# Performance work log

Measured on AMD Instinct MI355X. Metric: run time of the kernel, lower is better.

Reference implementation:

```python
import jax, jax.numpy as jnp
import numpy as np

IN_DIM = 4096
OUT_DIM = 2048
K = 4
R = 4096
B = 4096


def setup_inputs() -> dict:
    key = jax.random.key(0)
    ks = jax.random.split(key, 8)
    s = 0.02
    return {
        "hidden_states": jax.random.normal(ks[0], (B, IN_DIM), jnp.float32),
        # stacked per-block weights, torch Linear layout: W1/W3 [k+1, out, in], W2 [k+1, in, out]
        "W1": jax.random.normal(ks[1], (K + 1, OUT_DIM, IN_DIM), jnp.float32) * s,
        "W3": jax.random.normal(ks[2], (K + 1, OUT_DIM, IN_DIM), jnp.float32) * s,
        "W2": jax.random.normal(ks[3], (K + 1, IN_DIM, OUT_DIM), jnp.float32) * s,
        "fc1_w": jax.random.normal(ks[4], (R, IN_DIM * K), jnp.float32) * s,
        "fc1_b": jax.random.normal(ks[5], (R,), jnp.float32) * s,
        "fc2_w": jax.random.normal(ks[6], (IN_DIM, R), jnp.float32) * s,
        "fc2_b": jax.random.normal(ks[7], (IN_DIM,), jnp.float32) * s,
    }


def reference(hidden_states, W1, W3, W2, fc1_w, fc1_b, fc2_w, fc2_b):
    x = hidden_states
    # batched SwiGLU over k+1 blocks: [B, k+1, out]
    g = jax.nn.silu(jnp.einsum("bi,koi->bko", x, W1)) * jnp.einsum("bi,koi->bko", x, W3)
    wk_outs = jnp.einsum("bko,kio->bki", g, W2)  # [B, k+1, in]
    o0 = wk_outs[:, 0]                            # [B, in]
    concat = wk_outs[:, 1:].reshape(x.shape[0], -1)  # [B, k*in], matches torch.cat order
    h = jax.nn.silu(concat @ fc1_w.T + fc1_b)
    proj = h @ fc2_w.T + fc2_b                    # [B, in]
    diff = o0 - proj
    return (jnp.linalg.norm(diff, ord=2, axis=1), jnp.mean(jnp.abs(diff), axis=1))
```

## Files before the change

kernel.cpp:

```cpp
#include <hip/hip_runtime.h>
#include <hip/hip_bf16.h>
#include <cstdint>
#include <cstddef>

#define IN_DIM 4096
#define OUT_DIM 2048
#define NEXP 5
#define KEXP 4
#define RDIM 4096
#define BATCH 4096

typedef __hip_bfloat16 bf16;
typedef __attribute__((ext_vector_type(8))) short bf16x8;
typedef __attribute__((ext_vector_type(4))) float f32x4;
typedef __attribute__((ext_vector_type(8))) unsigned short u16x8;
typedef __attribute__((ext_vector_type(4))) unsigned short u16x4;

typedef const __attribute__((address_space(1))) unsigned int* as1p;
typedef __attribute__((address_space(3))) unsigned int* as3p;

__device__ __forceinline__ unsigned short f2bf(float x) {
  union { __hip_bfloat16 h; unsigned short u; } cv;
  cv.h = __float2bfloat16(x);
  return cv.u;
}

__global__ __launch_bounds__(256) void cvt_kernel(const float* __restrict__ in,
                                                  unsigned short* __restrict__ out,
                                                  int n8) {
  int i = blockIdx.x * 256 + threadIdx.x;
  if (i >= n8) return;
  const float4* p = (const float4*)in;
  float4 a = p[(size_t)i * 2];
  float4 b = p[(size_t)i * 2 + 1];
  u16x8 v;
  v[0] = f2bf(a.x); v[1] = f2bf(a.y); v[2] = f2bf(a.z); v[3] = f2bf(a.w);
  v[4] = f2bf(b.x); v[5] = f2bf(b.y); v[6] = f2bf(b.z); v[7] = f2bf(b.w);
  *(u16x8*)(out + (size_t)i * 8) = v;
}

__global__ __launch_bounds__(256) void tcvt_kernel(const float* __restrict__ in,
                                                   unsigned short* __restrict__ out,
                                                   int NI, int NO) {
  __shared__ float tile[32][33];
  const float* inz = in + (size_t)blockIdx.z * NI * NO;
  unsigned short* outz = out + (size_t)blockIdx.z * NI * NO;
  int i0 = blockIdx.y * 32;
  int o0 = blockIdx.x * 32;
  int t = threadIdx.x;
  int ri = t >> 3, ro = (t & 7) << 2;
  float4 v = *(const float4*)(inz + (size_t)(i0 + ri) * NO + o0 + ro);
  tile[ri][ro] = v.x; tile[ri][ro + 1] = v.y; tile[ri][ro + 2] = v.z; tile[ri][ro + 3] = v.w;
  __syncthreads();
  int wo = t >> 3, wi = (t & 7) << 2;
  u16x4 w;
  w[0] = f2bf(tile[wi][wo]);
  w[1] = f2bf(tile[wi + 1][wo]);
  w[2] = f2bf(tile[wi + 2][wo]);
  w[3] = f2bf(tile[wi + 3][wo]);
  *(u16x4*)(outz + (size_t)(o0 + wo) * NI + i0 + wi) = w;
}

__device__ __forceinline__ void gload16(const bf16* g, bf16* l) {
  __builtin_amdgcn_global_load_lds((as1p)g, (as3p)l, 16, 0, 0);
}

template <int N> __device__ __forceinline__ void vwait() {
  if constexpr (N == 0) asm volatile("s_waitcnt vmcnt(0)" ::: "memory");
  else if constexpr (N == 2) asm volatile("s_waitcnt vmcnt(2)" ::: "memory");
  else if constexpr (N == 4) asm volatile("s_waitcnt vmcnt(4)" ::: "memory");
}

#define READ_A(buf, mh)                                              \
  do {                                                               \
    const bf16* _pa = ldsA + (buf) * 16384 + (mh) * 8192;            \
    _Pragma("unroll") for (int m2 = 0; m2 < 4; ++m2) {               \
      afr[m2][0] = *(const bf16x8*)(_pa + aOff[m2]);                 \
      afr[m2][1] = *(const bf16x8*)(_pa + (aOff[m2] ^ 32));          \
    }                                                                \
  } while (0)

#define READ_B(buf, nh)                                              \
  do {                                                               \
    const bf16* _pb = ldsB + (buf) * 16384 + (nh) * 8192;            \
    _Pragma("unroll") for (int n2 = 0; n2 < 2; ++n2) {               \
      bfr[(nh) * 2 + n2][0] = *(const bf16x8*)(_pb + bOff[(nh) * 2 + n2]);        \
      bfr[(nh) * 2 + n2][1] = *(const bf16x8*)(_pb + (bOff[(nh) * 2 + n2] ^ 32)); \
    }                                                                \
  } while (0)

#define QMFMA(mh, nh)                                                            \
  do {                                                                           \
    __builtin_amdgcn_s_setprio(1);                                               \
    _Pragma("unroll") for (int m2 = 0; m2 < 4; ++m2) {                           \
      _Pragma("unroll") for (int n2 = 0; n2 < 2; ++n2) {                         \
        acc[(mh) * 4 + m2][(nh) * 2 + n2] = __builtin_amdgcn_mfma_f32_16x16x32_bf16( \
            afr[m2][0], bfr[(nh) * 2 + n2][0], acc[(mh) * 4 + m2][(nh) * 2 + n2], 0, 0, 0); \
        acc[(mh) * 4 + m2][(nh) * 2 + n2] = __builtin_amdgcn_mfma_f32_16x16x32_bf16( \
            afr[m2][1], bfr[(nh) * 2 + n2][1], acc[(mh) * 4 + m2][(nh) * 2 + n2], 0, 0, 0); \
      }                                                                          \
    }                                                                            \
    __builtin_amdgcn_s_setprio(0);                                               \
  } while (0)

#define BAR() __builtin_amdgcn_s_barrier()

template <int EPI>
__global__ __launch_bounds__(512, 2) void gemm8p(
    const bf16* __restrict__ A, int lda, long long aZ,
    const bf16* __restrict__ B, int ldb, long long bZ,
    int Kdim,
    unsigned short* __restrict__ C, int ldc, long long cZ,
    const float* __restrict__ bias,
    const bf16* __restrict__ AUX, int ldaux, long long auxZ,
    float* __restrict__ accum,
    int gx, int gxy, int nwg8) {
  extern __shared__ __align__(16) bf16 lds[];
  bf16* ldsA = lds;
  bf16* ldsB = lds + 32768;

  int flat = blockIdx.x;
  int wg = (flat & 7) * nwg8 + (flat >> 3);
  int z = wg / gxy;
  int r0 = wg - z * gxy;
  int by = r0 / gx;
  int bx = r0 - by * gx;
  int rowBase = by * 256, colBase = bx * 256;

  int tid = threadIdx.x;
  int wave = tid >> 6, lane = tid & 63;
  int wr = wave >> 2, wc = wave & 3;

  const bf16* Ab = A + (long long)z * aZ + (long long)rowBase * lda;
  const bf16* Bb = B + (long long)z * bZ + (long long)colBase * ldb;

  int rl = tid >> 3;
  int cg8 = ((tid & 7) ^ (rl & 7)) << 3;
  int srcA = rl * lda + cg8;
  int srcB = rl * ldb + cg8;
  int dstOfs = wave * 512;

  int aOff[4], bOff[4];
#pragma unroll
  for (int m2 = 0; m2 < 4; ++m2) {
    int rA = ((2 * m2 + wr) * 16) + (lane & 15);
    aOff[m2] = rA * 64 + (((lane >> 4) ^ (rA & 7)) << 3);
  }
#pragma unroll
  for (int n = 0; n < 4; ++n) {
    int rB = (((4 * n + wc) * 16) & 127) + (lane & 15);
    bOff[n] = rB * 64 + (((lane >> 4) ^ (rB & 7)) << 3);
  }

  f32x4 acc[8][4] = {};
  bf16x8 afr[4][2], bfr[4][2];

  auto stA = [&](int buf, int hh, int kt) {
    const bf16* s = Ab + (long long)(hh * 128) * lda + kt * 64;
    bf16* d = ldsA + buf * 16384 + hh * 8192 + dstOfs;
    gload16(s + srcA, d);
    gload16(s + srcA + 64 * lda, d + 4096);
  };
  auto stB = [&](int buf, int hh, int kt) {
    const bf16* s = Bb + (long long)(hh * 128) * ldb + kt * 64;
    bf16* d = ldsB + buf * 16384 + hh * 8192 + dstOfs;
    gload16(s + srcB, d);
    gload16(s + srcB + 64 * ldb, d + 4096);
  };

  int NT = Kdim >> 6;
  int cur = 0;

  stA(0, 0, 0); stB(0, 0, 0); stB(0, 1, 0); stA(0, 1, 0);
  vwait<4>();
  BAR();

  for (int t = 0; t < NT - 1; ++t) {
    int nb = cur ^ 1;
    READ_A(cur, 0);
    READ_B(cur, 0);
    stA(nb, 0, t + 1);
    vwait<4>();
    BAR();
    QMFMA(0, 0);
    READ_B(cur, 1);
    stB(nb, 0, t + 1);
    vwait<4>();
    BAR();
    QMFMA(0, 1);
    READ_A(cur, 1);
    stB(nb, 1, t + 1);
    BAR();
    QMFMA(1, 1);
    stA(nb, 1, t + 1);
    vwait<4>();
    BAR();
    QMFMA(1, 0);
    cur = nb;
  }

  READ_A(cur, 0);
  READ_B(cur, 0);
  vwait<2>();
  BAR();
  QMFMA(0, 0);
  READ_B(cur, 1);
  vwait<0>();
  BAR();
  QMFMA(0, 1);
  READ_A(cur, 1);
  QMFMA(1, 1);
  QMFMA(1, 0);

  if constexpr (EPI == 2) {
    const bf16* AUXb = AUX + (long long)z * auxZ;
#pragma unroll
    for (int m = 0; m < 8; ++m) {
#pragma unroll
      for (int r = 0; r < 4; ++r) {
        int row = rowBase + (2 * m + wr) * 16 + ((lane >> 4) << 2) + r;
        float ssq = 0.f, sab = 0.f;
#pragma unroll
        for (int n = 0; n < 4; ++n) {
          int col = colBase + (4 * n + wc) * 16 + (lane & 15);
          float p = acc[m][n][r] + bias[col];
          float d = __bfloat162float(AUXb[(long long)row * ldaux + col]) - p;
          ssq += d * d;
          sab += fabsf(d);
        }
#pragma unroll
        for (int off = 1; off < 16; off <<= 1) {
          ssq += __shfl_xor(ssq, off);
          sab += __shfl_xor(sab, off);
        }
        if ((lane & 15) == 0) {
          atomicAdd(&accum[row], ssq);
          atomicAdd(&accum[BATCH + row], sab);
        }
      }
    }
  } else {
    unsigned short* Cb = C + (long long)z * cZ;
    const bf16* AUXb = (EPI == 3) ? (AUX + (long long)z * auxZ) : nullptr;
#pragma unroll
    for (int m = 0; m < 8; ++m) {
#pragma unroll
      for (int n = 0; n < 4; ++n) {
        int col = colBase + (4 * n + wc) * 16 + (lane & 15);
#pragma unroll
        for (int r = 0; r < 4; ++r) {
          int row = rowBase + (2 * m + wr) * 16 + ((lane >> 4) << 2) + r;
          float v = acc[m][n][r];
          if constexpr (EPI == 1) {
            v += bias[col];
            v = v / (1.f + __expf(-v));
          } else if constexpr (EPI == 3) {
            float s = __bfloat162float(AUXb[(long long)row * ldaux + col]);
            v = v * (s / (1.f + __expf(-s)));
          }
          Cb[(long long)row * ldc + col] = f2bf(v);
        }
      }
    }
  }
}

__global__ void zero_accum(float* a) {
  int i = blockIdx.x * 256 + threadIdx.x;
  if (i < 2 * BATCH) a[i] = 0.f;
}

__global__ void finalize_kernel(const float* __restrict__ accum, float* __restrict__ out) {
  int b = blockIdx.x * 256 + threadIdx.x;
  if (b < BATCH) {
    out[b] = sqrtf(accum[b]);
    out[BATCH + b] = accum[BATCH + b] * (1.f / IN_DIM);
  }
}

extern "C" void kernel_launch(void* const* d_in, const int* in_sizes, int n_in,
                              void* d_out, int out_size, void* d_ws, size_t ws_size,
                              hipStream_t stream) {
  const float* x    = (const float*)d_in[0];
  const float* W1   = (const float*)d_in[1];
  const float* W3   = (const float*)d_in[2];
  const float* W2   = (const float*)d_in[3];
  const float* fc1w = (const float*)d_in[4];
  const float* fc1b = (const float*)d_in[5];
  const float* fc2w = (const float*)d_in[6];
  const float* fc2b = (const float*)d_in[7];
  float* out = (float*)d_out;

  char* ws = (char*)d_ws;
  size_t off = 0;
  auto alloc = [&](size_t bytes) {
    char* p = ws + off;
    off += (bytes + 255) & ~(size_t)255;
    return p;
  };
  bf16* xb   = (bf16*)alloc((size_t)BATCH * IN_DIM * 2);
  bf16* w1b  = (bf16*)alloc((size_t)NEXP * OUT_DIM * IN_DIM * 2);
  bf16* w3b  = (bf16*)alloc((size_t)NEXP * OUT_DIM * IN_DIM * 2);
  bf16* w2b0 = (bf16*)alloc((size_t)IN_DIM * OUT_DIM * 2);
  bf16* w2t  = (bf16*)alloc((size_t)KEXP * OUT_DIM * IN_DIM * 2);
  bf16* f1b  = (bf16*)alloc((size_t)RDIM * IN_DIM * KEXP * 2);
  bf16* f2b  = (bf16*)alloc((size_t)IN_DIM * RDIM * 2);
  bf16* gbuf = (bf16*)alloc((size_t)BATCH * NEXP * OUT_DIM * 2);
  bf16* t1   = (bf16*)alloc((size_t)BATCH * NEXP * OUT_DIM * 2);
  bf16* o0   = (bf16*)alloc((size_t)BATCH * IN_DIM * 2);
  bf16* hbuf = (bf16*)alloc((size_t)BATCH * RDIM * 2);
  float* accum = (float*)alloc((size_t)2 * BATCH * 4);
  if (off > ws_size) return;

  bf16* Pcat = t1;

  auto cvt = [&](const float* in, bf16* outp, size_t n) {
    int n8 = (int)(n / 8);
    cvt_kernel<<<(n8 + 255) / 256, 256, 0, stream>>>(in, (unsigned short*)outp, n8);
  };
  cvt(x,    xb,   (size_t)BATCH * IN_DIM);
  cvt(W1,   w1b,  (size_t)NEXP * OUT_DIM * IN_DIM);
  cvt(W3,   w3b,  (size_t)NEXP * OUT_DIM * IN_DIM);
  cvt(W2,   w2b0, (size_t)IN_DIM * OUT_DIM);
  cvt(fc1w, f1b,  (size_t)RDIM * IN_DIM * KEXP);
  cvt(fc2w, f2b,  (size_t)IN_DIM * RDIM);
  tcvt_kernel<<<dim3(OUT_DIM / 32, IN_DIM / 32, KEXP), 256, 0, stream>>>(
      W2 + (size_t)IN_DIM * OUT_DIM, (unsigned short*)w2t, IN_DIM, OUT_DIM);

  const size_t LDSB = 131072;

  {
    int gx = OUT_DIM / 256, gxy = gx * (BATCH / 256), nwg = gxy * NEXP;
    gemm8p<0><<<nwg, 512, LDSB, stream>>>(
        xb, IN_DIM, 0LL,
        w1b, IN_DIM, (long long)OUT_DIM * IN_DIM,
        IN_DIM,
        (unsigned short*)t1, NEXP * OUT_DIM, (long long)OUT_DIM,
        nullptr, nullptr, 0, 0LL, nullptr,
        gx, gxy, nwg / 8);
  }
  {
    int gx = OUT_DIM / 256, gxy = gx * (BATCH / 256), nwg = gxy * NEXP;
    gemm8p<3><<<nwg, 512, LDSB, stream>>>(
        xb, IN_DIM, 0LL,
        w3b, IN_DIM, (long long)OUT_DIM * IN_DIM,
        IN_DIM,
        (unsigned short*)gbuf, NEXP * OUT_DIM, (long long)OUT_DIM,
        nullptr, t1, NEXP * OUT_DIM, (long long)OUT_DIM, nullptr,
        gx, gxy, nwg / 8);
  }
  {
    int gx = IN_DIM / 256, gxy = gx * (BATCH / 256), nwg = gxy;
    gemm8p<0><<<nwg, 512, LDSB, stream>>>(
        gbuf, NEXP * OUT_DIM, 0LL,
        w2b0, OUT_DIM, 0LL,
        OUT_DIM,
        (unsigned short*)o0, IN_DIM, 0LL,
        nullptr, nullptr, 0, 0LL, nullptr,
        gx, gxy, nwg / 8);
  }
  {
    int gx = OUT_DIM / 256, gxy = gx * (RDIM / 256), nwg = gxy * KEXP;
    gemm8p<0><<<nwg, 512, LDSB, stream>>>(
        f1b, KEXP * IN_DIM, (long long)IN_DIM,
        w2t, IN_DIM, (long long)OUT_DIM * IN_DIM,
        IN_DIM,
        (unsigned short*)Pcat, KEXP * OUT_DIM, (long long)OUT_DIM,
        nullptr, nullptr, 0, 0LL, nullptr,
        gx, gxy, nwg / 8);
  }
  {
    int gx = RDIM / 256, gxy = gx * (BATCH / 256), nwg = gxy;
    gemm8p<1><<<nwg, 512, LDSB, stream>>>(
        gbuf + OUT_DIM, NEXP * OUT_DIM, 0LL,
        Pcat, KEXP * OUT_DIM, 0LL,
        KEXP * OUT_DIM,
        (unsigned short*)hbuf, RDIM, 0LL,
        fc1b, nullptr, 0, 0LL, nullptr,
        gx, gxy, nwg / 8);
  }
  zero_accum<<<(2 * BATCH + 255) / 256, 256, 0, stream>>>(accum);
  {
    int gx = IN_DIM / 256, gxy = gx * (BATCH / 256), nwg = gxy;
    gemm8p<2><<<nwg, 512, LDSB, stream>>>(
        hbuf, RDIM, 0LL,
        f2b, RDIM, 0LL,
        RDIM,
        nullptr, 0, 0LL,
        fc2b, o0, IN_DIM, 0LL, accum,
        gx, gxy, nwg / 8);
  }
  finalize_kernel<<<(BATCH + 255) / 256, 256, 0, stream>>>(accum, out);
}
```

Before: 1.447 ms.

## Deepen GEMM main loop prefetch with half-tile staggered loads across two buffers

Restructures the bf16 MFMA GEMM main loop into a two-iteration unrolled schedule where global-to-LDS loads for the next k-tiles are issued at quarter-tile granularity, roughly a full tile ahead. Waits use vmcnt(6) instead of vmcnt(4), so more loads stay in flight and fewer barriers block on memory. This aims to hide global memory latency better. It assumes an even number of k-tiles and relies on careful ordering of LDS buffer reuse, so a mistake in that ordering risks a race.

Result: slower. 1.488 ms (+2.8%).

```diff
diff --git a/kernel.cpp b/kernel.cpp
--- a/kernel.cpp
+++ b/kernel.cpp
@@ -69,6 +69,7 @@
   if constexpr (N == 0) asm volatile("s_waitcnt vmcnt(0)" ::: "memory");
   else if constexpr (N == 2) asm volatile("s_waitcnt vmcnt(2)" ::: "memory");
   else if constexpr (N == 4) asm volatile("s_waitcnt vmcnt(4)" ::: "memory");
+  else if constexpr (N == 6) asm volatile("s_waitcnt vmcnt(6)" ::: "memory");
 }
 
 #define READ_A(buf, mh)                                              \
@@ -169,47 +170,57 @@
   };
 
   int NT = Kdim >> 6;
-  int cur = 0;
+  int NP = NT >> 1;
 
   stA(0, 0, 0); stB(0, 0, 0); stB(0, 1, 0); stA(0, 1, 0);
-  vwait<4>();
-  BAR();
-
-  for (int t = 0; t < NT - 1; ++t) {
-    int nb = cur ^ 1;
-    READ_A(cur, 0);
-    READ_B(cur, 0);
-    stA(nb, 0, t + 1);
-    vwait<4>();
-    BAR();
+  stA(1, 0, 1); stB(1, 0, 1); stB(1, 1, 1);
+
+  for (int i = 0; i < NP - 1; ++i) {
+    int t = 2 * i;
+    vwait<6>(); BAR();
+    READ_A(0, 0); READ_B(0, 0);
+    stA(1, 1, t + 1);
     QMFMA(0, 0);
-    READ_B(cur, 1);
-    stB(nb, 0, t + 1);
-    vwait<4>();
-    BAR();
+    BAR();
+    READ_B(0, 1);
+    stA(0, 0, t + 2);
     QMFMA(0, 1);
-    READ_A(cur, 1);
-    stB(nb, 1, t + 1);
-    BAR();
+    BAR();
+    READ_A(0, 1);
+    stB(0, 0, t + 2);
     QMFMA(1, 1);
-    stA(nb, 1, t + 1);
-    vwait<4>();
-    BAR();
+    BAR();
+    stB(0, 1, t + 2);
     QMFMA(1, 0);
-    cur = nb;
-  }
-
-  READ_A(cur, 0);
-  READ_B(cur, 0);
-  vwait<2>();
-  BAR();
+    vwait<6>(); BAR();
+    READ_A(1, 0); READ_B(1, 0);
+    stA(0, 1, t + 2);
+    QMFMA(0, 0);
+    BAR();
+    READ_B(1, 1);
+    stA(1, 0, t + 3);
+    QMFMA(0, 1);
+    BAR();
+    READ_A(1, 1);
+    stB(1, 0, t + 3);
+    QMFMA(1, 1);
+    BAR();
+    stB(1, 1, t + 3);
+    QMFMA(1, 0);
+  }
+
+  vwait<6>(); BAR();
+  READ_A(0, 0); READ_B(0, 0);
+  stA(1, 1, NT - 1);
   QMFMA(0, 0);
-  READ_B(cur, 1);
-  vwait<0>();
-  BAR();
-  QMFMA(0, 1);
-  READ_A(cur, 1);
-  QMFMA(1, 1);
+  BAR(); READ_B(0, 1); QMFMA(0, 1);
+  BAR(); READ_A(0, 1); QMFMA(1, 1);
+  BAR(); QMFMA(1, 0);
+  vwait<0>(); BAR();
+  READ_A(1, 0); READ_B(1, 0);
+  QMFMA(0, 0);
+  BAR(); READ_B(1, 1); QMFMA(0, 1);
+  BAR(); READ_A(1, 1); QMFMA(1, 1);
   QMFMA(1, 0);
 
   if constexpr (EPI == 2) {
```

## Fuse W1 and W3 SwiGLU GEMMs into a single dual-accumulator kernel

Applied to the files above, without the earlier changes.

Replaces the two separate gate and up-projection GEMMs with one kernel that loads each A tile once and multiplies it against both W1 and W3 tiles. The SwiGLU epilogue is applied in registers. This removes the intermediate t1 buffer's write and read-back and halves the A-operand loads for this stage. In exchange the output tile narrows to 128 columns, doubles the accumulator register pressure, and uses a new hand-written LDS pipeline with different barrier placement.

After: 1.374 ms (median of 3 runs). 1.05x faster.

```diff
diff --git a/kernel.cpp b/kernel.cpp
--- a/kernel.cpp
+++ b/kernel.cpp
@@ -265,6 +265,165 @@
   }
 }
 
+#define READ_B1(buf)                                                  \
+  do {                                                                \
+    const bf16* _pb = ldsB1 + (buf) * 8192;                           \
+    _Pragma("unroll") for (int n2 = 0; n2 < 2; ++n2) {                \
+      b1fr[n2][0] = *(const bf16x8*)(_pb + bOff[n2]);                 \
+      b1fr[n2][1] = *(const bf16x8*)(_pb + (bOff[n2] ^ 32));          \
+    }                                                                 \
+  } while (0)
+
+#define READ_B3(buf)                                                  \
+  do {                                                                \
+    const bf16* _pb = ldsB3 + (buf) * 8192;                           \
+    _Pragma("unroll") for (int n2 = 0; n2 < 2; ++n2) {                \
+      b3fr[n2][0] = *(const bf16x8*)(_pb + bOff[n2]);                 \
+      b3fr[n2][1] = *(const bf16x8*)(_pb + (bOff[n2] ^ 32));          \
+    }                                                                 \
+  } while (0)
+
+#define QMFMA_D(ACC, mh, BF)                                                     \
+  do {                                                                           \
+    __builtin_amdgcn_s_setprio(1);                                               \
+    _Pragma("unroll") for (int m2 = 0; m2 < 4; ++m2) {                           \
+      _Pragma("unroll") for (int n2 = 0; n2 < 2; ++n2) {                         \
+        ACC[(mh) * 4 + m2][n2] = __builtin_amdgcn_mfma_f32_16x16x32_bf16(        \
+            afr[m2][0], BF[n2][0], ACC[(mh) * 4 + m2][n2], 0, 0, 0);             \
+        ACC[(mh) * 4 + m2][n2] = __builtin_amdgcn_mfma_f32_16x16x32_bf16(        \
+            afr[m2][1], BF[n2][1], ACC[(mh) * 4 + m2][n2], 0, 0, 0);             \
+      }                                                                          \
+    }                                                                            \
+    __builtin_amdgcn_s_setprio(0);                                               \
+  } while (0)
+
+__global__ __launch_bounds__(512, 2) void gemm_dual(
+    const bf16* __restrict__ A,
+    const bf16* __restrict__ W1b, const bf16* __restrict__ W3b,
+    unsigned short* __restrict__ G,
+    int gx, int gxy, int nwg8) {
+  extern __shared__ __align__(16) bf16 lds[];
+  bf16* ldsA = lds;
+  bf16* ldsB1 = lds + 32768;
+  bf16* ldsB3 = lds + 49152;
+
+  int flat = blockIdx.x;
+  int wg = (flat & 7) * nwg8 + (flat >> 3);
+  int z = wg / gxy;
+  int r0 = wg - z * gxy;
+  int by = r0 / gx;
+  int bx = r0 - by * gx;
+  int rowBase = by * 256, colBase = bx * 128;
+
+  int tid = threadIdx.x;
+  int wave = tid >> 6, lane = tid & 63;
+  int wr = wave >> 2, wc = wave & 3;
+
+  const bf16* Ab = A + (long long)rowBase * IN_DIM;
+  const bf16* B1b = W1b + (long long)z * OUT_DIM * IN_DIM + (long long)colBase * IN_DIM;
+  const bf16* B3b = W3b + (long long)z * OUT_DIM * IN_DIM + (long long)colBase * IN_DIM;
+
+  int rl = tid >> 3;
+  int cg8 = ((tid & 7) ^ (rl & 7)) << 3;
+  int src = rl * IN_DIM + cg8;
+  int dstOfs = wave * 512;
+
+  int aOff[4], bOff[2];
+#pragma unroll
+  for (int m2 = 0; m2 < 4; ++m2) {
+    int rA = ((2 * m2 + wr) * 16) + (lane & 15);
+    aOff[m2] = rA * 64 + (((lane >> 4) ^ (rA & 7)) << 3);
+  }
+#pragma unroll
+  for (int n2 = 0; n2 < 2; ++n2) {
+    int rB = (4 * n2 + wc) * 16 + (lane & 15);
+    bOff[n2] = rB * 64 + (((lane >> 4) ^ (rB & 7)) << 3);
+  }
+
+  f32x4 acc1[8][2] = {};
+  f32x4 acc2[8][2] = {};
+  bf16x8 afr[4][2], b1fr[2][2], b3fr[2][2];
+
+  auto stA = [&](int buf, int hh, int kt) {
+    const bf16* s = Ab + (long long)(hh * 128) * IN_DIM + kt * 64;
+    bf16* d = ldsA + buf * 16384 + hh * 8192 + dstOfs;
+    gload16(s + src, d);
+    gload16(s + src + 64 * IN_DIM, d + 4096);
+  };
+  auto stB1 = [&](int buf, int kt) {
+    const bf16* s = B1b + kt * 64;
+    bf16* d = ldsB1 + buf * 8192 + dstOfs;
+    gload16(s + src, d);
+    gload16(s + src + 64 * IN_DIM, d + 4096);
+  };
+  auto stB3 = [&](int buf, int kt) {
+    const bf16* s = B3b + kt * 64;
+    bf16* d = ldsB3 + buf * 8192 + dstOfs;
+    gload16(s + src, d);
+    gload16(s + src + 64 * IN_DIM, d + 4096);
+  };
+
+  const int NT = IN_DIM >> 6;
+  int cur = 0;
+
+  stA(0, 0, 0); stB1(0, 0); stB3(0, 0); stA(0, 1, 0);
+  vwait<4>();
+  BAR();
+
+  for (int t = 0; t < NT - 1; ++t) {
+    int nb = cur ^ 1;
+    READ_A(cur, 0);
+    READ_B1(cur);
+    stA(nb, 0, t + 1);
+    vwait<4>();
+    BAR();
+    QMFMA_D(acc1, 0, b1fr);
+    READ_B3(cur);
+    stB1(nb, t + 1);
+    vwait<4>();
+    BAR();
+    QMFMA_D(acc2, 0, b3fr);
+    READ_A(cur, 1);
+    stB3(nb, t + 1);
+    BAR();
+    QMFMA_D(acc1, 1, b1fr);
+    stA(nb, 1, t + 1);
+    vwait<4>();
+    BAR();
+    QMFMA_D(acc2, 1, b3fr);
+    cur = nb;
+  }
+
+  READ_A(cur, 0);
+  READ_B1(cur);
+  vwait<2>();
+  BAR();
+  QMFMA_D(acc1, 0, b1fr);
+  READ_B3(cur);
+  vwait<0>();
+  BAR();
+  QMFMA_D(acc2, 0, b3fr);
+  READ_A(cur, 1);
+  QMFMA_D(acc1, 1, b1fr);
+  QMFMA_D(acc2, 1, b3fr);
+
+  unsigned short* Gb = G + (long long)z * OUT_DIM;
+#pragma unroll
+  for (int m = 0; m < 8; ++m) {
+#pragma unroll
+    for (int n2 = 0; n2 < 2; ++n2) {
+      int col = colBase + (4 * n2 + wc) * 16 + (lane & 15);
+#pragma unroll
+      for (int r = 0; r < 4; ++r) {
+        int row = rowBase + (2 * m + wr) * 16 + ((lane >> 4) << 2) + r;
+        float v1 = acc1[m][n2][r], v2 = acc2[m][n2][r];
+        float g = v2 * (v1 / (1.f + __expf(-v1)));
+        Gb[(long long)row * (NEXP * OUT_DIM) + col] = f2bf(g);
+      }
+    }
+  }
+}
+
 __global__ void zero_accum(float* a) {
   int i = blockIdx.x * 256 + threadIdx.x;
   if (i < 2 * BATCH) a[i] = 0.f;
@@ -306,13 +465,13 @@
   bf16* f1b  = (bf16*)alloc((size_t)RDIM * IN_DIM * KEXP * 2);
   bf16* f2b  = (bf16*)alloc((size_t)IN_DIM * RDIM * 2);
   bf16* gbuf = (bf16*)alloc((size_t)BATCH * NEXP * OUT_DIM * 2);
-  bf16* t1   = (bf16*)alloc((size_t)BATCH * NEXP * OUT_DIM * 2);
+  bf16* scratch = (bf16*)alloc((size_t)RDIM * KEXP * OUT_DIM * 2);
   bf16* o0   = (bf16*)alloc((size_t)BATCH * IN_DIM * 2);
   bf16* hbuf = (bf16*)alloc((size_t)BATCH * RDIM * 2);
   float* accum = (float*)alloc((size_t)2 * BATCH * 4);
   if (off > ws_size) return;
 
-  bf16* Pcat = t1;
+  bf16* Pcat = scratch;
 
   auto cvt = [&](const float* in, bf16* outp, size_t n) {
     int n8 = (int)(n / 8);
@@ -330,24 +489,9 @@
   const size_t LDSB = 131072;
 
   {
-    int gx = OUT_DIM / 256, gxy = gx * (BATCH / 256), nwg = gxy * NEXP;
-    gemm8p<0><<<nwg, 512, LDSB, stream>>>(
-        xb, IN_DIM, 0LL,
-        w1b, IN_DIM, (long long)OUT_DIM * IN_DIM,
-        IN_DIM,
-        (unsigned short*)t1, NEXP * OUT_DIM, (long long)OUT_DIM,
-        nullptr, nullptr, 0, 0LL, nullptr,
-        gx, gxy, nwg / 8);
-  }
-  {
-    int gx = OUT_DIM / 256, gxy = gx * (BATCH / 256), nwg = gxy * NEXP;
-    gemm8p<3><<<nwg, 512, LDSB, stream>>>(
-        xb, IN_DIM, 0LL,
-        w3b, IN_DIM, (long long)OUT_DIM * IN_DIM,
-        IN_DIM,
-        (unsigned short*)gbuf, NEXP * OUT_DIM, (long long)OUT_DIM,
-        nullptr, t1, NEXP * OUT_DIM, (long long)OUT_DIM, nullptr,
-        gx, gxy, nwg / 8);
+    int gx = OUT_DIM / 128, gxy = gx * (BATCH / 256), nwg = gxy * NEXP;
+    gemm_dual<<<nwg, 512, LDSB, stream>>>(
+        xb, w1b, w3b, (unsigned short*)gbuf, gx, gxy, nwg / 8);
   }
   {
     int gx = IN_DIM / 256, gxy = gx * (BATCH / 256), nwg = gxy;
```
